# Kernel tuning notes

Measured on AMD Instinct MI355X. Metric: run time of the kernel, lower is better.

The kernel has to match this reference:

```python
import jax, jax.numpy as jnp
import numpy as np

N = 100000
E = 1600000
IN_DIM, H1, H2, H3 = 128, 128, 64, 32


def gcn_conv(x, edge_index, W, b, n):
    # PyG GCNConv (default): add self-loops, symmetric norm D^-1/2 (A+I) D^-1/2,
    # out[dst] = sum_{src->dst} norm * (x @ W)[src] + b
    src, dst = edge_index[0], edge_index[1]
    loops = jnp.arange(n)
    src = jnp.concatenate([src, loops])
    dst = jnp.concatenate([dst, loops])
    deg = jax.ops.segment_sum(jnp.ones((src.shape[0],), dtype=x.dtype), dst, num_segments=n)
    dinv = jnp.where(deg > 0, jax.lax.rsqrt(deg), jnp.zeros((), dtype=x.dtype))
    norm = dinv[src] * dinv[dst]  # [E+N]
    h = x @ W                      # [N, out_dim] dense transform first (out_dim <= in_dim)
    msg = h[src] * norm[:, None]   # [E+N, out_dim] gather + scale
    out = jax.ops.segment_sum(msg, dst, num_segments=n)
    return out + b


def setup_inputs() -> dict:
    key = jax.random.key(0)
    ks = jax.random.split(key, 10)
    def glorot(k, shape):
        lim = np.sqrt(6.0 / (shape[0] + shape[1]))
        return jax.random.uniform(k, shape, jnp.float32, -lim, lim)
    return {
        "x": jax.random.normal(ks[0], (N, IN_DIM), jnp.float32),
        "edge_index": jax.random.randint(ks[1], (2, E), 0, N, jnp.int64),
        "W1": glorot(ks[2], (IN_DIM, H1)), "b1": jnp.zeros((H1,), jnp.float32),
        "W2": glorot(ks[3], (H1, H2)),     "b2": jnp.zeros((H2,), jnp.float32),
        "W3": glorot(ks[4], (H2, H3)),     "b3": jnp.zeros((H3,), jnp.float32),
        "Wl": glorot(ks[5], (H3, 1)),      "bl": jnp.zeros((1,), jnp.float32),
    }


def reference(x, edge_index, W1, b1, W2, b2, W3, b3, Wl, bl):
    n = x.shape[0]
    h = jax.nn.relu(gcn_conv(x, edge_index, W1, b1, n))   # dropout p=0.5 is identity in eval
    h = jax.nn.relu(gcn_conv(h, edge_index, W2, b2, n))
    h = jax.nn.relu(gcn_conv(h, edge_index, W3, b3, n))
    return jax.nn.sigmoid(h @ Wl + bl)                    # [N, 1]
```

## Files before the change

kernel.cpp:

```cpp
#include <hip/hip_runtime.h>
#include <hip/hip_fp16.h>
#include <math.h>


#define BSHIFT 8
#define BNODES (1 << BSHIFT)
#define SRCBITS 17
#define MAXB 512

union H8 { float4 f4; __half2 h2[4]; };

typedef _Float16 half8 __attribute__((ext_vector_type(8)));
typedef float floatx4 __attribute__((ext_vector_type(4)));


__global__ __launch_bounds__(256) void k_hist(const int* __restrict__ dst, int E,
                                              int* __restrict__ bucketcnt, int B) {
    __shared__ int h[MAXB];
    int tid = threadIdx.x;
    h[tid] = 0; h[tid + 256] = 0;
    __syncthreads();
    for (int i = blockIdx.x * 256 + tid; i < E; i += gridDim.x * 256)
        atomicAdd(&h[dst[i] >> BSHIFT], 1);
    __syncthreads();
    if (tid < B && h[tid] > 0) atomicAdd(&bucketcnt[tid], h[tid]);
    int t2 = tid + 256;
    if (t2 < B && h[t2] > 0) atomicAdd(&bucketcnt[t2], h[t2]);
}

__global__ __launch_bounds__(512) void k_bscan(const int* __restrict__ bucketcnt,
                                               int* __restrict__ bucketbase,
                                               int* __restrict__ bucketfill,
                                               int* __restrict__ row_ptr,
                                               int B, int n, int E) {
    __shared__ int s[MAXB];
    int tid = threadIdx.x;
    int v = (tid < B) ? bucketcnt[tid] : 0;
    s[tid] = v;
    __syncthreads();
    for (int off = 1; off < MAXB; off <<= 1) {
        int t = (tid >= off) ? s[tid - off] : 0;
        __syncthreads();
        s[tid] += t;
        __syncthreads();
    }
    int excl = s[tid] - v;
    if (tid < B) { bucketbase[tid] = excl; bucketfill[tid] = excl; }
    if (tid == 0) { bucketbase[B] = E; row_ptr[n] = E; }
}

__global__ __launch_bounds__(256) void k_bucket(const int* __restrict__ src,
                                                const int* __restrict__ dst, int E,
                                                int* __restrict__ bucketfill,
                                                unsigned int* __restrict__ edgebuf,
                                                int B) {
    __shared__ int h[MAXB];
    __shared__ int cursor[MAXB];
    int tid = threadIdx.x;
    int base = blockIdx.x * 4096;
    int end = min(base + 4096, E);
    h[tid] = 0; h[tid + 256] = 0;
    __syncthreads();
    for (int i = base + tid; i < end; i += 256)
        atomicAdd(&h[dst[i] >> BSHIFT], 1);
    __syncthreads();
    if (tid < B) cursor[tid] = (h[tid] > 0) ? atomicAdd(&bucketfill[tid], h[tid]) : 0;
    int t2 = tid + 256;
    if (t2 < B) cursor[t2] = (h[t2] > 0) ? atomicAdd(&bucketfill[t2], h[t2]) : 0;
    __syncthreads();
    for (int i = base + tid; i < end; i += 256) {
        int d = dst[i];
        int b = d >> BSHIFT;
        unsigned int pk = ((unsigned int)(d & (BNODES - 1)) << SRCBITS) | (unsigned int)src[i];
        int pos = atomicAdd(&cursor[b], 1);
        edgebuf[pos] = pk;
    }
}

__global__ __launch_bounds__(256) void k_build(const unsigned int* __restrict__ edgebuf,
                                               const int* __restrict__ bucketbase,
                                               int* __restrict__ row_ptr,
                                               float* __restrict__ dinv,
                                               int* __restrict__ col, int n) {
    __shared__ int cnt[BNODES];
    __shared__ int s[BNODES];
    int b = blockIdx.x;
    int tid = threadIdx.x;
    int node0 = b << BSHIFT;
    int ebase = bucketbase[b], eend = bucketbase[b + 1];
    cnt[tid] = 0;
    __syncthreads();
    for (int i = ebase + tid; i < eend; i += 256)
        atomicAdd(&cnt[edgebuf[i] >> SRCBITS], 1);
    __syncthreads();
    int c = cnt[tid];
    s[tid] = c;
    __syncthreads();
    for (int off = 1; off < 256; off <<= 1) {
        int t = (tid >= off) ? s[tid - off] : 0;
        __syncthreads();
        s[tid] += t;
        __syncthreads();
    }
    int p = ebase + s[tid] - c;
    int node = node0 + tid;
    if (node < n) { row_ptr[node] = p; dinv[node] = rsqrtf((float)(c + 1)); }
    cnt[tid] = p;
    __syncthreads();
    for (int i = ebase + tid; i < eend; i += 256) {
        unsigned int pk = edgebuf[i];
        int pos = atomicAdd(&cnt[pk >> SRCBITS], 1);
        col[pos] = (int)(pk & ((1u << SRCBITS) - 1));
    }
}

__global__ void k_packW3(const float* __restrict__ W1, const float* __restrict__ W2,
                         const float* __restrict__ W3, _Float16* __restrict__ P1,
                         _Float16* __restrict__ P2, _Float16* __restrict__ P3) {
    int e = blockIdx.x * 256 + threadIdx.x;
    const float* W; _Float16* P; int OUT, idx;
    if (e < 16384)      { W = W1; P = P1; OUT = 128; idx = e; }
    else if (e < 24576) { W = W2; P = P2; OUT = 64;  idx = e - 16384; }
    else if (e < 26624) { W = W3; P = P3; OUT = 32;  idx = e - 24576; }
    else return;
    int j = idx & 7;
    int lane = (idx >> 3) & 63;
    int rest = idx >> 9;
    int NT = OUT >> 4;
    int t = rest % NT;
    int ss = rest / NT;
    int k = ss * 32 + (lane >> 4) * 8 + j;
    int nn = t * 16 + (lane & 15);
    P[idx] = (_Float16)W[k * OUT + nn];
}

template <int IN, int OUT>
__global__ __launch_bounds__(256) void k_matmul_mfma(const float* __restrict__ x,
                                                     const _Float16* __restrict__ Wpk,
                                                     const float* __restrict__ dinv,
                                                     __half* __restrict__ out, int n) {
    constexpr int S = IN / 32;
    constexpr int NT = OUT / 16;
    constexpr int LDH = IN + 8;
    __shared__ _Float16 xs[64 * LDH];

    int tid = threadIdx.x;
    int rowbase = blockIdx.x * 64;

    constexpr int TOT = 64 * IN / 8;
    const float4* x4 = (const float4*)x;
    for (int i = tid; i < TOT; i += 256) {
        int r = i / (IN / 8), kg = i % (IN / 8);
        int row = rowbase + r;
        float4 a = make_float4(0.f, 0.f, 0.f, 0.f), b = a;
        if (row < n) {
            a = x4[(size_t)row * (IN / 4) + kg * 2 + 0];
            b = x4[(size_t)row * (IN / 4) + kg * 2 + 1];
        }
        _Float16* p = &xs[r * LDH + kg * 8];
        p[0] = (_Float16)a.x; p[1] = (_Float16)a.y;
        p[2] = (_Float16)a.z; p[3] = (_Float16)a.w;
        p[4] = (_Float16)b.x; p[5] = (_Float16)b.y;
        p[6] = (_Float16)b.z; p[7] = (_Float16)b.w;
    }
    __syncthreads();

    int lane = tid & 63;
    int wave = tid >> 6;
    int m = lane & 15, quad = lane >> 4;

    floatx4 acc[NT];
#pragma unroll
    for (int t = 0; t < NT; ++t) acc[t] = (floatx4){0.f, 0.f, 0.f, 0.f};

    const half8* Wf = (const half8*)Wpk;
#pragma unroll
    for (int s = 0; s < S; ++s) {
        half8 a = *(const half8*)&xs[(wave * 16 + m) * LDH + s * 32 + quad * 8];
#pragma unroll
        for (int t = 0; t < NT; ++t) {
            half8 b = Wf[(s * NT + t) * 64 + lane];
            acc[t] = __builtin_amdgcn_mfma_f32_16x16x32_f16(a, b, acc[t], 0, 0, 0);
        }
    }

    int rbase = rowbase + wave * 16 + quad * 4;
#pragma unroll
    for (int r = 0; r < 4; ++r) {
        int row = rbase + r;
        if (row < n) {
            float dsc = dinv[row];
#pragma unroll
            for (int t = 0; t < NT; ++t)
                out[(size_t)row * OUT + t * 16 + m] = __float2half(acc[t][r] * dsc);
        }
    }
}

template <int F, int OUT>
__global__ __launch_bounds__(256) void k_agg_mm(const __half* __restrict__ hs,
                                                const float* __restrict__ dinv,
                                                const float* __restrict__ bias,
                                                const int* __restrict__ row_ptr,
                                                const int* __restrict__ col,
                                                const _Float16* __restrict__ Wpk,
                                                __half* __restrict__ out, int n) {
    constexpr int S = F / 32;
    constexpr int NT = OUT / 16;
    constexpr int LDH = F + 8;
    constexpr int LPN = F / 8;
    __shared__ _Float16 zs[64 * LDH];

    int tid = threadIdx.x;
    int rowbase = blockIdx.x * 64;
    const float4* h4 = (const float4*)hs;

    for (int task = tid; task < 64 * LPN; task += 256) {
        int nl = task / LPN;
        int fg = task % LPN;
        int node = rowbase + nl;
        H8 o;
        if (node < n) {
            float acc[8];
            H8 u;
            u.f4 = h4[(size_t)node * LPN + fg];
#pragma unroll
            for (int q = 0; q < 4; ++q) {
                float2 f = __half22float2(u.h2[q]);
                acc[2 * q + 0] = f.x;
                acc[2 * q + 1] = f.y;
            }
            int beg = row_ptr[node], end = row_ptr[node + 1];
            int j = beg;
            for (; j + 3 < end; j += 4) {
                int s0 = col[j], s1 = col[j + 1], s2 = col[j + 2], s3 = col[j + 3];
                H8 u0, u1, u2, u3;
                u0.f4 = h4[(size_t)s0 * LPN + fg];
                u1.f4 = h4[(size_t)s1 * LPN + fg];
                u2.f4 = h4[(size_t)s2 * LPN + fg];
                u3.f4 = h4[(size_t)s3 * LPN + fg];
#pragma unroll
                for (int q = 0; q < 4; ++q) {
                    float2 f0 = __half22float2(u0.h2[q]);
                    float2 f1 = __half22float2(u1.h2[q]);
                    float2 f2 = __half22float2(u2.h2[q]);
                    float2 f3 = __half22float2(u3.h2[q]);
                    acc[2 * q + 0] += (f0.x + f1.x) + (f2.x + f3.x);
                    acc[2 * q + 1] += (f0.y + f1.y) + (f2.y + f3.y);
                }
            }
            for (; j < end; ++j) {
                H8 u2;
                u2.f4 = h4[(size_t)col[j] * LPN + fg];
#pragma unroll
                for (int q = 0; q < 4; ++q) {
                    float2 f = __half22float2(u2.h2[q]);
                    acc[2 * q + 0] += f.x;
                    acc[2 * q + 1] += f.y;
                }
            }
            float dsc = dinv[node];
#pragma unroll
            for (int q = 0; q < 4; ++q) {
                float v0 = fmaxf(fmaf(acc[2 * q + 0], dsc, bias[fg * 8 + 2 * q + 0]), 0.f);
                float v1 = fmaxf(fmaf(acc[2 * q + 1], dsc, bias[fg * 8 + 2 * q + 1]), 0.f);
                o.h2[q] = __floats2half2_rn(v0, v1);
            }
        } else {
            o.f4 = make_float4(0.f, 0.f, 0.f, 0.f);
        }
        *(float4*)&zs[nl * LDH + fg * 8] = o.f4;
    }
    __syncthreads();

    int lane = tid & 63;
    int wave = tid >> 6;
    int m = lane & 15, quad = lane >> 4;

    floatx4 acc[NT];
#pragma unroll
    for (int t = 0; t < NT; ++t) acc[t] = (floatx4){0.f, 0.f, 0.f, 0.f};

    const half8* Wf = (const half8*)Wpk;
#pragma unroll
    for (int s = 0; s < S; ++s) {
        half8 a = *(const half8*)&zs[(wave * 16 + m) * LDH + s * 32 + quad * 8];
#pragma unroll
        for (int t = 0; t < NT; ++t) {
            half8 b = Wf[(s * NT + t) * 64 + lane];
            acc[t] = __builtin_amdgcn_mfma_f32_16x16x32_f16(a, b, acc[t], 0, 0, 0);
        }
    }

    int rbase = rowbase + wave * 16 + quad * 4;
#pragma unroll
    for (int r = 0; r < 4; ++r) {
        int row = rbase + r;
        if (row < n) {
            float dsc = dinv[row];
#pragma unroll
            for (int t = 0; t < NT; ++t)
                out[(size_t)row * OUT + t * 16 + m] = __float2half(acc[t][r] * dsc);
        }
    }
}

__global__ __launch_bounds__(256) void k_agg_final(const __half* __restrict__ hs,
                                                   const float* __restrict__ dinv,
                                                   const float* __restrict__ bias,
                                                   const int* __restrict__ row_ptr,
                                                   const int* __restrict__ col,
                                                   const float* __restrict__ Wl,
                                                   const float* __restrict__ bl,
                                                   float* __restrict__ out, int n) {
    constexpr int LPN = 4;
    int t = blockIdx.x * 256 + threadIdx.x;
    int node = t / LPN;
    int fg = t % LPN;
    if (node >= n) return;

    const float4* h4 = (const float4*)hs;
    float acc[8];
    {
        H8 u;
        u.f4 = h4[(size_t)node * LPN + fg];
#pragma unroll
        for (int q = 0; q < 4; ++q) {
            float2 f = __half22float2(u.h2[q]);
            acc[2 * q + 0] = f.x;
            acc[2 * q + 1] = f.y;
        }
    }
    int beg = row_ptr[node], end = row_ptr[node + 1];
    int j = beg;
    for (; j + 3 < end; j += 4) {
        int s0 = col[j], s1 = col[j + 1], s2 = col[j + 2], s3 = col[j + 3];
        H8 u0, u1, u2, u3;
        u0.f4 = h4[(size_t)s0 * LPN + fg];
        u1.f4 = h4[(size_t)s1 * LPN + fg];
        u2.f4 = h4[(size_t)s2 * LPN + fg];
        u3.f4 = h4[(size_t)s3 * LPN + fg];
#pragma unroll
        for (int q = 0; q < 4; ++q) {
            float2 f0 = __half22float2(u0.h2[q]);
            float2 f1 = __half22float2(u1.h2[q]);
            float2 f2 = __half22float2(u2.h2[q]);
            float2 f3 = __half22float2(u3.h2[q]);
            acc[2 * q + 0] += (f0.x + f1.x) + (f2.x + f3.x);
            acc[2 * q + 1] += (f0.y + f1.y) + (f2.y + f3.y);
        }
    }
    for (; j < end; ++j) {
        H8 u;
        u.f4 = h4[(size_t)col[j] * LPN + fg];
#pragma unroll
        for (int q = 0; q < 4; ++q) {
            float2 f = __half22float2(u.h2[q]);
            acc[2 * q + 0] += f.x;
            acc[2 * q + 1] += f.y;
        }
    }
    float dsc = dinv[node];
    float partial = 0.f;
#pragma unroll
    for (int k = 0; k < 8; ++k) {
        float v = fmaxf(fmaf(acc[k], dsc, bias[fg * 8 + k]), 0.f);
        partial = fmaf(v, Wl[fg * 8 + k], partial);
    }
    partial += __shfl_xor(partial, 1);
    partial += __shfl_xor(partial, 2);
    if (fg == 0) out[node] = 1.f / (1.f + expf(-(partial + bl[0])));
}

extern "C" void kernel_launch(void* const* d_in, const int* in_sizes, int n_in,
                              void* d_out, int out_size, void* d_ws, size_t ws_size,
                              hipStream_t stream) {
    const float* x  = (const float*)d_in[0];
    const int*   ei = (const int*)d_in[1];
    const float* W1 = (const float*)d_in[2];
    const float* b1 = (const float*)d_in[3];
    const float* W2 = (const float*)d_in[4];
    const float* b2 = (const float*)d_in[5];
    const float* W3 = (const float*)d_in[6];
    const float* b3 = (const float*)d_in[7];
    const float* Wl = (const float*)d_in[8];
    const float* bl = (const float*)d_in[9];

    const int N = in_sizes[0] / 128;
    const int E = in_sizes[1] / 2;
    const int* src = ei;
    const int* dst = ei + E;
    const int B = (N + BNODES - 1) >> BSHIFT;

    char* ws = (char*)d_ws;
    size_t off = 0;
    auto take = [&](size_t bytes) -> char* {
        char* p = ws + off;
        off += (bytes + 255) & ~(size_t)255;
        return p;
    };
    int*          bucketcnt  = (int*)take(MAXB * 4);
    int*          bucketbase = (int*)take((MAXB + 1) * 4);
    int*          bucketfill = (int*)take(MAXB * 4);
    unsigned int* edgebuf    = (unsigned int*)take((size_t)E * 4);
    int*          row_ptr    = (int*)take((size_t)(N + 1) * 4);
    float*        dinv       = (float*)take((size_t)N * 4);
    int*          col        = (int*)take((size_t)E * 4);
    __half*       bufA       = (__half*)take((size_t)N * 128 * 2);
    __half*       bufB       = (__half*)take((size_t)N * 128 * 2);
    _Float16*     Wpk1       = (_Float16*)take(128 * 128 * 2);
    _Float16*     Wpk2       = (_Float16*)take(128 * 64 * 2);
    _Float16*     Wpk3       = (_Float16*)take(64 * 32 * 2);
    (void)ws_size;

    hipMemsetAsync(bucketcnt, 0, MAXB * 4, stream);

    int gM = (N + 63) / 64;

    k_hist<<<512, 256, 0, stream>>>(dst, E, bucketcnt, B);
    k_bscan<<<1, MAXB, 0, stream>>>(bucketcnt, bucketbase, bucketfill, row_ptr, B, N, E);
    k_bucket<<<(E + 4095) / 4096, 256, 0, stream>>>(src, dst, E, bucketfill, edgebuf, B);
    k_build<<<B, 256, 0, stream>>>(edgebuf, bucketbase, row_ptr, dinv, col, N);

    k_packW3<<<(26624 + 255) / 256, 256, 0, stream>>>(W1, W2, W3, Wpk1, Wpk2, Wpk3);

    k_matmul_mfma<128, 128><<<gM, 256, 0, stream>>>(x, Wpk1, dinv, bufA, N);

    k_agg_mm<128, 64><<<gM, 256, 0, stream>>>(bufA, dinv, b1, row_ptr, col, Wpk2, bufB, N);

    k_agg_mm<64, 32><<<gM, 256, 0, stream>>>(bufB, dinv, b2, row_ptr, col, Wpk3, bufA, N);

    k_agg_final<<<((size_t)N * 4 + 255) / 256, 256, 0, stream>>>(
        bufA, dinv, b3, row_ptr, col, Wl, bl, (float*)d_out, N);
}
```

Measured before the change: 295.0 us.

## Replace global-atomic bucket sort with per-chunk histogram matrix and column scan

The bucketing step now has each 16K-edge chunk write its per-bucket counts to a count matrix. A column scan per bucket turns those counts into per-chunk offsets, so the scatter pass no longer recomputes the local histogram or takes global atomic reservations on bucketfill, and the memset goes away. This costs an extra kernel launch and a count matrix read and written through global memory. The scan assumes at most 256 chunks. Separately, the fp16 conversion in the matmul staging now packs half2 pairs and does one vector store to LDS.

New measurement: 297.9 us. Within noise of the previous version (+1.0%).

```diff
diff --git a/kernel.cpp b/kernel.cpp
--- a/kernel.cpp
+++ b/kernel.cpp
@@ -7,35 +7,52 @@
 #define BNODES (1 << BSHIFT)
 #define SRCBITS 17
 #define MAXB 512
+#define CHUNK 16384
 
 union H8 { float4 f4; __half2 h2[4]; };
 
 typedef _Float16 half8 __attribute__((ext_vector_type(8)));
 typedef float floatx4 __attribute__((ext_vector_type(4)));
 
-
-__global__ __launch_bounds__(256) void k_hist(const int* __restrict__ dst, int E,
-                                              int* __restrict__ bucketcnt, int B) {
+__global__ __launch_bounds__(256) void k_hist2(const int* __restrict__ dst, int E,
+                                               int* __restrict__ cnt_mat, int B) {
     __shared__ int h[MAXB];
-    int tid = threadIdx.x;
+    int tid = threadIdx.x, c = blockIdx.x;
     h[tid] = 0; h[tid + 256] = 0;
     __syncthreads();
-    for (int i = blockIdx.x * 256 + tid; i < E; i += gridDim.x * 256)
+    int base = c * CHUNK, end = min(base + CHUNK, E);
+    for (int i = base + tid; i < end; i += 256)
         atomicAdd(&h[dst[i] >> BSHIFT], 1);
     __syncthreads();
-    if (tid < B && h[tid] > 0) atomicAdd(&bucketcnt[tid], h[tid]);
-    int t2 = tid + 256;
-    if (t2 < B && h[t2] > 0) atomicAdd(&bucketcnt[t2], h[t2]);
-}
-
-__global__ __launch_bounds__(512) void k_bscan(const int* __restrict__ bucketcnt,
+    for (int b = tid; b < B; b += 256) cnt_mat[c * B + b] = h[b];
+}
+
+__global__ __launch_bounds__(256) void k_colscan(const int* __restrict__ cnt_mat,
+                                                 int* __restrict__ rel_mat,
+                                                 int* __restrict__ total,
+                                                 int B, int nchunks) {
+    __shared__ int s[256];
+    int b = blockIdx.x, tid = threadIdx.x;
+    int v = (tid < nchunks) ? cnt_mat[tid * B + b] : 0;
+    s[tid] = v;
+    __syncthreads();
+    for (int off = 1; off < 256; off <<= 1) {
+        int t = (tid >= off) ? s[tid - off] : 0;
+        __syncthreads();
+        s[tid] += t;
+        __syncthreads();
+    }
+    if (tid < nchunks) rel_mat[tid * B + b] = s[tid] - v;
+    if (tid == 255) total[b] = s[255];
+}
+
+__global__ __launch_bounds__(512) void k_bscan(const int* __restrict__ total,
                                                int* __restrict__ bucketbase,
-                                               int* __restrict__ bucketfill,
                                                int* __restrict__ row_ptr,
                                                int B, int n, int E) {
     __shared__ int s[MAXB];
     int tid = threadIdx.x;
-    int v = (tid < B) ? bucketcnt[tid] : 0;
+    int v = (tid < B) ? total[tid] : 0;
     s[tid] = v;
     __syncthreads();
     for (int off = 1; off < MAXB; off <<= 1) {
@@ -44,35 +61,26 @@
         s[tid] += t;
         __syncthreads();
     }
-    int excl = s[tid] - v;
-    if (tid < B) { bucketbase[tid] = excl; bucketfill[tid] = excl; }
+    if (tid < B) bucketbase[tid] = s[tid] - v;
     if (tid == 0) { bucketbase[B] = E; row_ptr[n] = E; }
 }
 
-__global__ __launch_bounds__(256) void k_bucket(const int* __restrict__ src,
-                                                const int* __restrict__ dst, int E,
-                                                int* __restrict__ bucketfill,
-                                                unsigned int* __restrict__ edgebuf,
-                                                int B) {
-    __shared__ int h[MAXB];
-    __shared__ int cursor[MAXB];
-    int tid = threadIdx.x;
-    int base = blockIdx.x * 4096;
-    int end = min(base + 4096, E);
-    h[tid] = 0; h[tid + 256] = 0;
-    __syncthreads();
-    for (int i = base + tid; i < end; i += 256)
-        atomicAdd(&h[dst[i] >> BSHIFT], 1);
-    __syncthreads();
-    if (tid < B) cursor[tid] = (h[tid] > 0) ? atomicAdd(&bucketfill[tid], h[tid]) : 0;
-    int t2 = tid + 256;
-    if (t2 < B) cursor[t2] = (h[t2] > 0) ? atomicAdd(&bucketfill[t2], h[t2]) : 0;
+__global__ __launch_bounds__(256) void k_bucket2(const int* __restrict__ src,
+                                                 const int* __restrict__ dst, int E,
+                                                 const int* __restrict__ bucketbase,
+                                                 const int* __restrict__ rel_mat,
+                                                 unsigned int* __restrict__ edgebuf,
+                                                 int B) {
+    __shared__ int cur[MAXB];
+    int c = blockIdx.x, tid = threadIdx.x;
+    int base = c * CHUNK, end = min(base + CHUNK, E);
+    for (int b = tid; b < B; b += 256) cur[b] = bucketbase[b] + rel_mat[c * B + b];
     __syncthreads();
     for (int i = base + tid; i < end; i += 256) {
         int d = dst[i];
         int b = d >> BSHIFT;
         unsigned int pk = ((unsigned int)(d & (BNODES - 1)) << SRCBITS) | (unsigned int)src[i];
-        int pos = atomicAdd(&cursor[b], 1);
+        int pos = atomicAdd(&cur[b], 1);
         edgebuf[pos] = pk;
     }
 }
@@ -157,11 +165,12 @@
             a = x4[(size_t)row * (IN / 4) + kg * 2 + 0];
             b = x4[(size_t)row * (IN / 4) + kg * 2 + 1];
         }
-        _Float16* p = &xs[r * LDH + kg * 8];
-        p[0] = (_Float16)a.x; p[1] = (_Float16)a.y;
-        p[2] = (_Float16)a.z; p[3] = (_Float16)a.w;
-        p[4] = (_Float16)b.x; p[5] = (_Float16)b.y;
-        p[6] = (_Float16)b.z; p[7] = (_Float16)b.w;
+        H8 u;
+        u.h2[0] = __float22half2_rn(make_float2(a.x, a.y));
+        u.h2[1] = __float22half2_rn(make_float2(a.z, a.w));
+        u.h2[2] = __float22half2_rn(make_float2(b.x, b.y));
+        u.h2[3] = __float22half2_rn(make_float2(b.z, b.w));
+        *(float4*)&xs[r * LDH + kg * 8] = u.f4;
     }
     __syncthreads();
 
@@ -391,6 +400,7 @@
     const int* src = ei;
     const int* dst = ei + E;
     const int B = (N + BNODES - 1) >> BSHIFT;
+    const int NC = (E + CHUNK - 1) / CHUNK;
 
     char* ws = (char*)d_ws;
     size_t off = 0;
@@ -399,9 +409,10 @@
         off += (bytes + 255) & ~(size_t)255;
         return p;
     };
-    int*          bucketcnt  = (int*)take(MAXB * 4);
+    int*          cnt_mat    = (int*)take((size_t)NC * B * 4);
+    int*          rel_mat    = (int*)take((size_t)NC * B * 4);
+    int*          total      = (int*)take(MAXB * 4);
     int*          bucketbase = (int*)take((MAXB + 1) * 4);
-    int*          bucketfill = (int*)take(MAXB * 4);
     unsigned int* edgebuf    = (unsigned int*)take((size_t)E * 4);
     int*          row_ptr    = (int*)take((size_t)(N + 1) * 4);
     float*        dinv       = (float*)take((size_t)N * 4);
@@ -413,13 +424,12 @@
     _Float16*     Wpk3       = (_Float16*)take(64 * 32 * 2);
     (void)ws_size;
 
-    hipMemsetAsync(bucketcnt, 0, MAXB * 4, stream);
-
     int gM = (N + 63) / 64;
 
-    k_hist<<<512, 256, 0, stream>>>(dst, E, bucketcnt, B);
-    k_bscan<<<1, MAXB, 0, stream>>>(bucketcnt, bucketbase, bucketfill, row_ptr, B, N, E);
-    k_bucket<<<(E + 4095) / 4096, 256, 0, stream>>>(src, dst, E, bucketfill, edgebuf, B);
+    k_hist2<<<NC, 256, 0, stream>>>(dst, E, cnt_mat, B);
+    k_colscan<<<B, 256, 0, stream>>>(cnt_mat, rel_mat, total, B, NC);
+    k_bscan<<<1, MAXB, 0, stream>>>(total, bucketbase, row_ptr, B, N, E);
+    k_bucket2<<<NC, 256, 0, stream>>>(src, dst, E, bucketbase, rel_mat, edgebuf, B);
     k_build<<<B, 256, 0, stream>>>(edgebuf, bucketbase, row_ptr, dinv, col, N);
 
     k_packW3<<<(26624 + 255) / 256, 256, 0, stream>>>(W1, W2, W3, Wpk1, Wpk2, Wpk3);
```
